# Kernel optimization log

Hardware: AMD Instinct MI355X
Metric: run time of the kernel (lower is better)

## Reference

```python
import jax, jax.numpy as jnp
import numpy as np

N = 20000   # atoms
E = 320000  # edges
G = 500     # molecules
D = 256     # node embedding depth
M = 128     # message depth
H = 4       # attention heads
DH = M // H
NR = 32     # radial basis functions
L = 4       # graph convolutions
T = 100     # atom types
EMB = 32    # atom type embedding dim
OUT = 512   # bottleneck dim
CUT = 6.0   # convolution cutoff (Angstrom)


def seg_softmax(logits, seg, num):
    m = jax.ops.segment_max(logits, seg, num_segments=num)
    e = jnp.exp(logits - m[seg])
    s = jax.ops.segment_sum(e, seg, num_segments=num)
    return e / (s[seg] + 1e-12)


def layernorm(x, eps=1e-5):
    mu = x.mean(-1, keepdims=True)
    var = ((x - mu) ** 2).mean(-1, keepdims=True)
    return (x - mu) * jax.lax.rsqrt(var + eps)


def setup_inputs() -> dict:
    key = jax.random.key(0)
    ks = jax.random.split(key, 20)
    s = 0.05
    pos = jax.random.normal(ks[0], (N, 3), dtype=jnp.float32) * 3.0
    z = jax.random.randint(ks[1], (N,), 0, T, dtype=jnp.int32)
    batch = jnp.sort(jax.random.randint(ks[2], (N,), 0, G, dtype=jnp.int32))
    edge_index = jax.random.randint(ks[3], (2, E), 0, N, dtype=jnp.int32)
    return {
        'pos': pos, 'z': z, 'batch': batch, 'edge_index': edge_index,
        'emb_table': jax.random.normal(ks[4], (T, EMB)) * s,
        'W_in': jax.random.normal(ks[5], (EMB + 3, D)) * s,
        'b_in': jnp.zeros((D,)),
        'Wq': jax.random.normal(ks[6], (L, D, M)) * s,
        'Wk': jax.random.normal(ks[7], (L, D, M)) * s,
        'Wv': jax.random.normal(ks[8], (L, D, M)) * s,
        'W_rbf': jax.random.normal(ks[9], (L, NR, M)) * s,
        'W_msg': jax.random.normal(ks[10], (L, M, D)) * s,
        'W_vgate': jax.random.normal(ks[11], (L, M, D)) * s,
        'W_vs': jax.random.normal(ks[12], (L, D, D)) * s,
        'W_node': jax.random.normal(ks[13], (L, D, D)) * s,
        'b_node': jnp.zeros((L, D)),
        'gamma': jnp.ones((L, D)),
        'w_att': jax.random.normal(ks[14], (D,)) * s,
        'W_out': jax.random.normal(ks[15], (D, OUT)) * s,
        'b_out': jnp.zeros((OUT,)),
    }


def reference(pos, z, batch, edge_index, emb_table, W_in, b_in, Wq, Wk, Wv,
              W_rbf, W_msg, W_vgate, W_vs, W_node, b_node, gamma, w_att,
              W_out, b_out):
    n = pos.shape[0]
    src, dst = edge_index[0], edge_index[1]
    # node init: atom-type embedding concat position -> linear
    h = jnp.concatenate([emb_table[z], pos], axis=-1) @ W_in + b_in  # [N,D]
    vfeat = jnp.zeros((n, 3, D), dtype=h.dtype)  # equivariant vector track
    # edge geometry + Bessel radial basis with cosine cutoff envelope
    rvec = pos[src] - pos[dst]                      # [E,3]
    dist = jnp.sqrt((rvec ** 2).sum(-1) + 1e-12)    # [E]
    unit = rvec / dist[:, None]
    freqs = jnp.arange(1, NR + 1, dtype=h.dtype) * (jnp.pi / CUT)
    env = jnp.where(dist < CUT, 0.5 * (jnp.cos(jnp.pi * dist / CUT) + 1.0), 0.0)
    rbf = jnp.sin(dist[:, None] * freqs) / dist[:, None] * env[:, None]  # [E,NR]
    inv_sqrt_dh = 1.0 / jnp.sqrt(jnp.asarray(DH, h.dtype))
    for l in range(L):
        ew = rbf @ W_rbf[l]                                   # [E,M] radial filter
        q = (h @ Wq[l])[dst].reshape(-1, H, DH)               # [E,H,DH]
        k = (h @ Wk[l])[src].reshape(-1, H, DH)
        vv = ((h @ Wv[l])[src] * ew).reshape(-1, H, DH)       # rbf-gated values
        logit = (q * k).sum(-1) * inv_sqrt_dh                 # [E,H]
        att = seg_softmax(logit, dst, n)                      # neighbor softmax per dest node
        me = (att[..., None] * vv).reshape(-1, M)             # [E,M] edge messages
        msg = jax.ops.segment_sum(me, dst, num_segments=n)    # [N,M]
        gate = me @ W_vgate[l]                                # [E,D]
        vfeat = vfeat + jax.ops.segment_sum(unit[:, :, None] * gate[:, None, :], dst, num_segments=n)
        upd = jax.nn.gelu(msg @ W_msg[l])                     # message -> node width
        upd = jax.nn.gelu(upd @ W_node[l] + b_node[l])        # nodewise FC layer
        vnorm = jnp.sqrt((vfeat ** 2).sum(1) + 1e-8)          # invariant vector norms [N,D]
        h = layernorm(h + upd + vnorm @ W_vs[l]) * gamma[l]
    # softmax graph aggregator -> bottleneck
    a = seg_softmax(h @ w_att, batch, G)                      # [N]
    pooled = jax.ops.segment_sum(a[:, None] * h, batch, num_segments=G)  # [G,D]
    return pooled @ W_out + b_out                             # [G,OUT]
```

## Files before the change

### kernel.cpp

```cpp
#include <hip/hip_runtime.h>
#include <math.h>

typedef unsigned char  u8;
typedef unsigned short u16;
typedef unsigned int   u32;
typedef __attribute__((ext_vector_type(8))) unsigned short ushort8;
typedef __attribute__((ext_vector_type(4))) unsigned short ushort4v;
typedef __attribute__((ext_vector_type(8))) short short8v;
typedef __attribute__((ext_vector_type(4))) float f32x4;
typedef __attribute__((ext_vector_type(2))) float f32x2;

__device__ __forceinline__ float gelu_f(float x) {
    const float c = 0.7978845608028654f;
    float x3 = x * x * x;
    float t = tanhf(c * (x + 0.044715f * x3));
    return 0.5f * x * (1.0f + t);
}

__device__ __forceinline__ u16 f2b(float f) {
    u32 u = __float_as_uint(f);
    return (u16)((u + 0x7FFFu + ((u >> 16) & 1u)) >> 16);
}
__device__ __forceinline__ float b2f(u16 u) {
    return __uint_as_float(((u32)u) << 16);
}

__device__ __forceinline__ u32 f2fp8_sw(float f) {
    u32 u = __float_as_uint(f);
    u32 s = (u >> 31) << 7;
    float af = fabsf(f);
    if (af >= 448.0f) return s | 0x7E;
    if (af < 0.015625f) {
        int m = __float2int_rn(af * 512.0f);
        if (m >= 8) return s | 0x08;
        return s | (u32)m;
    }
    u32 a = __float_as_uint(af);
    u32 r = a + 0xFFFFFu + ((a >> 20) & 1u);
    int e8 = (int)(r >> 23) - 120;
    u32 m3 = (r >> 20) & 7u;
    if (e8 >= 16) return s | 0x7E;
    return s | ((u32)e8 << 3) | m3;
}
__device__ __forceinline__ float fp8d_sw(u32 b) {
    u32 lo = b & 0x7Fu;
    u32 nb = (lo << 20) + 0x3C000000u;
    float n = __uint_as_float(nb | ((b & 0x80u) << 24));
    float sub = (float)(b & 7u) * 0.001953125f;
    sub = (b & 0x80u) ? -sub : sub;
    return (lo & 0x78u) ? n : sub;
}
__device__ __forceinline__ u8 f2fp8(float v) {
#if __has_builtin(__builtin_amdgcn_cvt_pk_fp8_f32)
    return (u8)(__builtin_amdgcn_cvt_pk_fp8_f32(v, v, 0, false) & 0xFF);
#else
    return (u8)f2fp8_sw(v);
#endif
}
__device__ __forceinline__ f32x2 kvdec(u32 pair) {
#if __has_builtin(__builtin_amdgcn_cvt_pk_f32_fp8)
    return __builtin_amdgcn_cvt_pk_f32_fp8((int)pair, false);
#else
    f32x2 r;
    r[0] = fp8d_sw(pair & 0xFF);
    r[1] = fp8d_sw((pair >> 8) & 0xFF);
    return r;
#endif
}

__device__ __forceinline__ void split_bf16(float f, u16& h, u16& l) {
    u32 u = __float_as_uint(f);
    u32 r = (u + 0x7FFFu + ((u >> 16) & 1u)) >> 16;
    h = (u16)r;
    float hf = __uint_as_float(r << 16);
    float d = f - hf;
    u32 u2 = __float_as_uint(d);
    l = (u16)((u2 + 0x7FFFu + ((u2 >> 16) & 1u)) >> 16);
}

__device__ __forceinline__ int xcd_swz(int orig, int nwg) {
    int q8 = nwg >> 3, r8 = nwg & 7;
    int xcd = orig & 7, ii = orig >> 3;
    return (xcd < r8 ? xcd * (q8 + 1) : r8 * (q8 + 1) + (xcd - r8) * q8) + ii;
}

__global__ __launch_bounds__(256) void zero2_i32(int* __restrict__ a, int na,
                                                 int* __restrict__ b, int nb) {
    int i = blockIdx.x * 256 + threadIdx.x;
    if (i < na) a[i] = 0;
    else if (i - na < nb) b[i - na] = 0;
}

struct TEntry { const float* src; u16* dh; u16* dl; int K; int N; };
struct TDesc  { TEntry e[29]; };

__global__ __launch_bounds__(256) void transpose_split(TDesc desc) {
    __shared__ float tile[32][33];
    TEntry en = desc.e[blockIdx.y];
    int tk = en.K >> 5, tn = en.N >> 5;
    int bx = blockIdx.x;
    if (bx >= tk * tn) return;
    int k0 = (bx % tk) * 32, n0 = (bx / tk) * 32;
    int tx = threadIdx.x & 31, ty = threadIdx.x >> 5;
    #pragma unroll
    for (int yy = 0; yy < 32; yy += 8)
        tile[ty + yy][tx] = en.src[(size_t)(k0 + ty + yy) * en.N + (n0 + tx)];
    __syncthreads();
    #pragma unroll
    for (int yy = 0; yy < 32; yy += 8) {
        int n = n0 + ty + yy, k = k0 + tx;
        float f = tile[tx][ty + yy];
        u16 h, l;
        split_bf16(f, h, l);
        en.dh[(size_t)n * en.K + k] = h;
        en.dl[(size_t)n * en.K + k] = l;
    }
}

__global__ __launch_bounds__(128) void build_rbf_table(
    const float* __restrict__ W_rbf, float* __restrict__ table)
{
    int k = blockIdx.x, l = blockIdx.y, m = threadIdx.x;
    const float* Wrbf_l = W_rbf + (size_t)l * 32 * 128;
    float* tbl = table + (size_t)l * 4098 * 128;
    const float PI = 3.14159265358979323846f;
    float d = fmaxf((float)k * (6.0f / 4096.0f), 1e-9f);
    float th = d * (PI / 6.0f);
    float s1, c1;
    __sincosf(th, &s1, &c1);
    float env = (d < 6.0f) ? (0.5f * c1 + 0.5f) : 0.0f;
    float invd = 1.0f / d;
    float two_c = 2.0f * c1;
    float sp = 0.f, sc = s1, dot = 0.f;
    #pragma unroll
    for (int r = 0; r < 32; ++r) {
        dot = fmaf(sc, Wrbf_l[r * 128 + m], dot);
        float sn = fmaf(two_c, sc, -sp);
        sp = sc; sc = sn;
    }
    tbl[(size_t)k * 128 + m] = dot * invd * env;
}

template<int OMODE, bool ACCUM, bool BIAS, bool DOGELU, bool SPLITB>
__global__ __launch_bounds__(256) void mfma_gemm(
    const u16* __restrict__ A, const u16* __restrict__ BH,
    const u16* __restrict__ BL, const float* __restrict__ bias,
    void* __restrict__ Cv, void* __restrict__ Cv2,
    int Mrows, int K, int Nc, int gx)
{
    constexpr bool STAGE_OUT = (OMODE == 1 || OMODE == 2);
    constexpr int MAIN_B = 128 * 40 * 2 * (SPLITB ? 3 : 2);
    constexpr int OUT_B  = STAGE_OUT ? 128 * 136 * 2 : 0;
    constexpr int SMEM_B = (MAIN_B > OUT_B) ? MAIN_B : OUT_B;
    __shared__ __align__(16) char smem[SMEM_B];
    u16 (*sA)[40]  = (u16(*)[40])smem;
    u16 (*sBh)[40] = (u16(*)[40])(smem + 128 * 40 * 2);
    u16 (*sBl)[40] = (u16(*)[40])(smem + 2 * 128 * 40 * 2);
    u16 (*sOut)[136] = (u16(*)[136])smem;

    const int wg = xcd_swz(blockIdx.x, gridDim.x);
    const int r0 = (wg / gx) * 128, c0 = (wg % gx) * 128;

    const int t = threadIdx.x;
    const int lane = t & 63, wid = t >> 6;
    const int wr = (wid >> 1) * 64, wc = (wid & 1) * 64;

    f32x4 acc[4][4] = {};

    const int srow = t >> 1;
    const int skc  = (t & 1) * 16;

    for (int k0 = 0; k0 < K; k0 += 32) {
        {
            int gr = r0 + srow;
            ushort8 h0, h1;
            if (gr < Mrows) {
                const u16* p = A + (size_t)gr * K + (k0 + skc);
                h0 = *(const ushort8*)p;
                h1 = *(const ushort8*)(p + 8);
            } else {
                #pragma unroll
                for (int j = 0; j < 8; ++j) { h0[j] = 0; h1[j] = 0; }
            }
            *(ushort8*)&sA[srow][skc]     = h0;
            *(ushort8*)&sA[srow][skc + 8] = h1;
        }
        {
            int cg = c0 + srow;
            const u16* ph = BH + (size_t)cg * K + (k0 + skc);
            *(ushort8*)&sBh[srow][skc]     = *(const ushort8*)(ph);
            *(ushort8*)&sBh[srow][skc + 8] = *(const ushort8*)(ph + 8);
            if constexpr (SPLITB) {
                const u16* pl = BL + (size_t)cg * K + (k0 + skc);
                *(ushort8*)&sBl[srow][skc]     = *(const ushort8*)(pl);
                *(ushort8*)&sBl[srow][skc + 8] = *(const ushort8*)(pl + 8);
            }
        }
        __syncthreads();

        const int arow = wr + (lane & 15);
        const int koff = (lane >> 4) * 8;
        short8v ah[4];
        #pragma unroll
        for (int fr = 0; fr < 4; ++fr)
            ah[fr] = *(const short8v*)&sA[arow + fr * 16][koff];
        #pragma unroll
        for (int fc = 0; fc < 4; ++fc) {
            int bcol = wc + fc * 16 + (lane & 15);
            short8v bh = *(const short8v*)&sBh[bcol][koff];
            #pragma unroll
            for (int fr = 0; fr < 4; ++fr)
                acc[fr][fc] = __builtin_amdgcn_mfma_f32_16x16x32_bf16(ah[fr], bh, acc[fr][fc], 0, 0, 0);
            if constexpr (SPLITB) {
                short8v bl = *(const short8v*)&sBl[bcol][koff];
                #pragma unroll
                for (int fr = 0; fr < 4; ++fr)
                    acc[fr][fc] = __builtin_amdgcn_mfma_f32_16x16x32_bf16(ah[fr], bl, acc[fr][fc], 0, 0, 0);
            }
        }
        __syncthreads();
    }

    if constexpr (STAGE_OUT) {
        #pragma unroll
        for (int fr = 0; fr < 4; ++fr) {
            int rbase = wr + fr * 16 + (lane >> 4) * 4;
            #pragma unroll
            for (int fc = 0; fc < 4; ++fc) {
                int col = wc + fc * 16 + (lane & 15);
                #pragma unroll
                for (int reg = 0; reg < 4; ++reg) {
                    float v = acc[fr][fc][reg];
                    if (BIAS)   v += bias[c0 + col];
                    if (DOGELU) v = gelu_f(v);
                    sOut[rbase + reg][col] = f2b(v);
                }
            }
        }
        __syncthreads();
        #pragma unroll
        for (int p = 0; p < 4; ++p) {
            int row = p * 32 + (t >> 3);
            int cch = (t & 7) * 16;
            int gr = r0 + row;
            if (gr < Mrows) {
                u16* gp = (u16*)Cv + (size_t)gr * Nc + c0 + cch;
                ushort8 v0 = *(ushort8*)&sOut[row][cch];
                ushort8 v1 = *(ushort8*)&sOut[row][cch + 8];
                if (OMODE == 2) {
                    ushort8 o0 = *(const ushort8*)gp;
                    ushort8 o1 = *(const ushort8*)(gp + 8);
                    #pragma unroll
                    for (int j = 0; j < 8; ++j) {
                        v0[j] = f2b(b2f(v0[j]) + b2f(o0[j]));
                        v1[j] = f2b(b2f(v1[j]) + b2f(o1[j]));
                    }
                }
                *(ushort8*)gp       = v0;
                *(ushort8*)(gp + 8) = v1;
            }
        }
    } else {
        #pragma unroll
        for (int fr = 0; fr < 4; ++fr) {
            int rbase = r0 + wr + fr * 16 + (lane >> 4) * 4;
            #pragma unroll
            for (int fc = 0; fc < 4; ++fc) {
                int col = c0 + wc + fc * 16 + (lane & 15);
                #pragma unroll
                for (int reg = 0; reg < 4; ++reg) {
                    int gr = rbase + reg;
                    if (gr >= Mrows) continue;
                    float v = acc[fr][fc][reg];
                    if (BIAS)   v += bias[col];
                    if (DOGELU) v = gelu_f(v);
                    if (OMODE == 0) {
                        float* pc = (float*)Cv + (size_t)gr * Nc + col;
                        if (ACCUM) v += *pc;
                        *pc = v;
                    } else {
                        if (col < 128)
                            ((u16*)Cv)[(size_t)gr * 128 + col] = f2b(v);
                        else if (col < 256)
                            ((u8*)Cv2)[(size_t)gr * 256 + (col - 128) * 2] = f2fp8(v);
                        else
                            ((u8*)Cv2)[(size_t)gr * 256 + (col - 256) * 2 + 1] = f2fp8(v);
                    }
                }
            }
        }
    }
}

__global__ __launch_bounds__(512) void mlp_kernel(
    const u16* __restrict__ msg, const u16* __restrict__ Wmsg,
    const u16* __restrict__ WndH, const u16* __restrict__ WndL,
    const float* __restrict__ bnd, u16* __restrict__ b2out, int Mrows)
{
    __shared__ __align__(16) u16 b1[128][264];
    __shared__ __align__(16) char sbuf[256 * 40 * 2 * 2];
    u16 (*sA)[40]   = (u16(*)[40])sbuf;
    u16 (*sB)[40]   = (u16(*)[40])(sbuf + 128 * 40 * 2);
    u16 (*sBh)[40]  = (u16(*)[40])sbuf;
    u16 (*sBl)[40]  = (u16(*)[40])(sbuf + 256 * 40 * 2);
    u16 (*sOut)[136] = (u16(*)[136])sbuf;

    const int r0 = xcd_swz(blockIdx.x, gridDim.x) * 128;
    const int t = threadIdx.x;
    const int lane = t & 63, wid = t >> 6;
    const int wr = (wid >> 2) * 64, wc = (wid & 3) * 64;

    f32x4 acc[4][4] = {};
    const int srowA = t >> 2, skcA = (t & 3) * 8;
    const int srowB = t >> 1, skcB = (t & 1) * 16;

    for (int k0 = 0; k0 < 128; k0 += 32) {
        {
            int gr = r0 + srowA;
            ushort8 h0;
            #pragma unroll
            for (int j = 0; j < 8; ++j) h0[j] = 0;
            if (gr < Mrows) h0 = *(const ushort8*)(msg + (size_t)gr * 128 + k0 + skcA);
            *(ushort8*)&sA[srowA][skcA] = h0;
        }
        {
            const u16* p = Wmsg + (size_t)srowB * 128 + k0 + skcB;
            *(ushort8*)&sB[srowB][skcB]     = *(const ushort8*)p;
            *(ushort8*)&sB[srowB][skcB + 8] = *(const ushort8*)(p + 8);
        }
        __syncthreads();
        const int arow = wr + (lane & 15);
        const int koff = (lane >> 4) * 8;
        short8v ah[4];
        #pragma unroll
        for (int fr = 0; fr < 4; ++fr)
            ah[fr] = *(const short8v*)&sA[arow + fr * 16][koff];
        #pragma unroll
        for (int fc = 0; fc < 4; ++fc) {
            int bcol = wc + fc * 16 + (lane & 15);
            short8v bh = *(const short8v*)&sB[bcol][koff];
            #pragma unroll
            for (int fr = 0; fr < 4; ++fr)
                acc[fr][fc] = __builtin_amdgcn_mfma_f32_16x16x32_bf16(ah[fr], bh, acc[fr][fc], 0, 0, 0);
        }
        __syncthreads();
    }
    #pragma unroll
    for (int fr = 0; fr < 4; ++fr) {
        int rbase = wr + fr * 16 + (lane >> 4) * 4;
        #pragma unroll
        for (int fc = 0; fc < 4; ++fc) {
            int col = wc + fc * 16 + (lane & 15);
            #pragma unroll
            for (int reg = 0; reg < 4; ++reg) {
                b1[rbase + reg][col] = f2b(gelu_f(acc[fr][fc][reg]));
                acc[fr][fc][reg] = 0.0f;
            }
        }
    }
    __syncthreads();

    for (int k0 = 0; k0 < 256; k0 += 32) {
        {
            const u16* ph = WndH + (size_t)srowB * 256 + k0 + skcB;
            const u16* pl = WndL + (size_t)srowB * 256 + k0 + skcB;
            *(ushort8*)&sBh[srowB][skcB]     = *(const ushort8*)ph;
            *(ushort8*)&sBh[srowB][skcB + 8] = *(const ushort8*)(ph + 8);
            *(ushort8*)&sBl[srowB][skcB]     = *(const ushort8*)pl;
            *(ushort8*)&sBl[srowB][skcB + 8] = *(const ushort8*)(pl + 8);
        }
        __syncthreads();
        const int arow = wr + (lane & 15);
        const int koff = (lane >> 4) * 8;
        short8v ah[4];
        #pragma unroll
        for (int fr = 0; fr < 4; ++fr)
            ah[fr] = *(const short8v*)&b1[arow + fr * 16][k0 + koff];
        #pragma unroll
        for (int fc = 0; fc < 4; ++fc) {
            int bcol = wc + fc * 16 + (lane & 15);
            short8v bh = *(const short8v*)&sBh[bcol][koff];
            short8v bl = *(const short8v*)&sBl[bcol][koff];
            #pragma unroll
            for (int fr = 0; fr < 4; ++fr) {
                acc[fr][fc] = __builtin_amdgcn_mfma_f32_16x16x32_bf16(ah[fr], bh, acc[fr][fc], 0, 0, 0);
                acc[fr][fc] = __builtin_amdgcn_mfma_f32_16x16x32_bf16(ah[fr], bl, acc[fr][fc], 0, 0, 0);
            }
        }
        __syncthreads();
    }

    #pragma unroll
    for (int fr = 0; fr < 4; ++fr) {
        int rbase = wr + fr * 16 + (lane >> 4) * 4;
        #pragma unroll
        for (int fc = 0; fc < 4; ++fc) {
            int col = wc + fc * 16 + (lane & 15);
            #pragma unroll
            for (int reg = 0; reg < 4; ++reg)
                sOut[rbase + reg][col] = f2b(gelu_f(acc[fr][fc][reg] + bnd[col]));
        }
    }
    __syncthreads();
    #pragma unroll
    for (int p = 0; p < 2; ++p) {
        int row = p * 64 + (t >> 3);
        int cch = (t & 7) * 16;
        int gr = r0 + row;
        if (gr < Mrows) {
            u16* gp = b2out + (size_t)gr * 256 + cch;
            *(ushort8*)gp       = *(ushort8*)&sOut[row][cch];
            *(ushort8*)(gp + 8) = *(ushort8*)&sOut[row][cch + 8];
        }
    }
}

__global__ __launch_bounds__(512) void vs_ln_kernel(
    const u16* __restrict__ vf, const u16* __restrict__ BH,
    const u16* __restrict__ BL, const u16* __restrict__ b2,
    const float* __restrict__ gamma_l, u16* __restrict__ h16, int Mrows)
{
    __shared__ __align__(16) u16 sA [128][40];
    __shared__ __align__(16) u16 sBh[256][40];
    __shared__ __align__(16) u16 sBl[256][40];
    __shared__ float sSum[128][4];
    __shared__ float sSq [128][4];

    const int r0 = blockIdx.x * 128;
    const int t = threadIdx.x;
    const int lane = t & 63, wid = t >> 6;
    const int wr = (wid >> 2) * 64, wc = (wid & 3) * 64;

    f32x4 acc[4][4] = {};
    const int K = 256;
    const int srow = t >> 2;
    const int skc  = (t & 3) * 8;

    for (int k0 = 0; k0 < K; k0 += 32) {
        {
            int gr = r0 + srow;
            ushort8 h0;
            #pragma unroll
            for (int j = 0; j < 8; ++j) h0[j] = 0;
            if (gr < Mrows) {
                const u16* base = vf + ((size_t)gr * 3) * 256 + k0 + skc;
                ushort8 v0 = *(const ushort8*)(base);
                ushort8 v1 = *(const ushort8*)(base + 256);
                ushort8 v2 = *(const ushort8*)(base + 512);
                #pragma unroll
                for (int j = 0; j < 8; ++j) {
                    float a = b2f(v0[j]), b = b2f(v1[j]), c = b2f(v2[j]);
                    h0[j] = f2b(sqrtf(a * a + b * b + c * c + 1e-8f));
                }
            }
            *(ushort8*)&sA[srow][skc] = h0;
        }
        {
            *(ushort8*)&sBh[srow][skc]       = *(const ushort8*)(BH + (size_t)srow * K + k0 + skc);
            *(ushort8*)&sBh[srow + 128][skc] = *(const ushort8*)(BH + (size_t)(srow + 128) * K + k0 + skc);
            *(ushort8*)&sBl[srow][skc]       = *(const ushort8*)(BL + (size_t)srow * K + k0 + skc);
            *(ushort8*)&sBl[srow + 128][skc] = *(const ushort8*)(BL + (size_t)(srow + 128) * K + k0 + skc);
        }
        __syncthreads();

        const int arow = wr + (lane & 15);
        const int koff = (lane >> 4) * 8;
        short8v ah[4];
        #pragma unroll
        for (int fr = 0; fr < 4; ++fr)
            ah[fr] = *(const short8v*)&sA[arow + fr * 16][koff];
        #pragma unroll
        for (int fc = 0; fc < 4; ++fc) {
            int bcol = wc + fc * 16 + (lane & 15);
            short8v bh = *(const short8v*)&sBh[bcol][koff];
            short8v bl = *(const short8v*)&sBl[bcol][koff];
            #pragma unroll
            for (int fr = 0; fr < 4; ++fr) {
                acc[fr][fc] = __builtin_amdgcn_mfma_f32_16x16x32_bf16(ah[fr], bh, acc[fr][fc], 0, 0, 0);
                acc[fr][fc] = __builtin_amdgcn_mfma_f32_16x16x32_bf16(ah[fr], bl, acc[fr][fc], 0, 0, 0);
            }
        }
        __syncthreads();
    }

    float psum[4][4] = {}, psq[4][4] = {};
    #pragma unroll
    for (int fr = 0; fr < 4; ++fr) {
        #pragma unroll
        for (int fc = 0; fc < 4; ++fc) {
            int col = wc + fc * 16 + (lane & 15);
            #pragma unroll
            for (int reg = 0; reg < 4; ++reg) {
                int gr = r0 + wr + fr * 16 + (lane >> 4) * 4 + reg;
                float x = 0.f;
                if (gr < Mrows) {
                    size_t ix = (size_t)gr * 256 + col;
                    x = acc[fr][fc][reg] + b2f(b2[ix]) + b2f(h16[ix]);
                }
                acc[fr][fc][reg] = x;
                psum[fr][reg] += x;
                psq[fr][reg]  = fmaf(x, x, psq[fr][reg]);
            }
        }
    }
    #pragma unroll
    for (int fr = 0; fr < 4; ++fr) {
        #pragma unroll
        for (int reg = 0; reg < 4; ++reg) {
            float s = psum[fr][reg], sq = psq[fr][reg];
            #pragma unroll
            for (int off = 8; off; off >>= 1) {
                s  += __shfl_xor(s, off);
                sq += __shfl_xor(sq, off);
            }
            psum[fr][reg] = s; psq[fr][reg] = sq;
        }
    }
    if ((lane & 15) == 0) {
        int qg = lane >> 4;
        #pragma unroll
        for (int fr = 0; fr < 4; ++fr) {
            #pragma unroll
            for (int reg = 0; reg < 4; ++reg) {
                int row = wr + fr * 16 + qg * 4 + reg;
                sSum[row][wc >> 6] = psum[fr][reg];
                sSq [row][wc >> 6] = psq[fr][reg];
            }
        }
    }
    __syncthreads();
    #pragma unroll
    for (int fr = 0; fr < 4; ++fr) {
        #pragma unroll
        for (int reg = 0; reg < 4; ++reg) {
            int row = wr + fr * 16 + (lane >> 4) * 4 + reg;
            int gr = r0 + row;
            if (gr >= Mrows) continue;
            float S = sSum[row][0] + sSum[row][1] + sSum[row][2] + sSum[row][3];
            float Q = sSq[row][0] + sSq[row][1] + sSq[row][2] + sSq[row][3];
            float mu = S * (1.0f / 256.0f);
            float var = fmaxf(Q * (1.0f / 256.0f) - mu * mu, 0.0f);
            float rs = rsqrtf(var + 1e-5f);
            #pragma unroll
            for (int fc = 0; fc < 4; ++fc) {
                int col = wc + fc * 16 + (lane & 15);
                float y = (acc[fr][fc][reg] - mu) * rs * gamma_l[col];
                h16[(size_t)gr * 256 + col] = f2b(y);
            }
        }
    }
}

__global__ __launch_bounds__(256) void setup_edges(
    const int* __restrict__ ei, const int* __restrict__ batch,
    const float* __restrict__ pos, int E_, int Nn,
    int* __restrict__ deg, int* __restrict__ gcnt, float4* __restrict__ eg)
{
    int x = blockIdx.x * 256 + threadIdx.x;
    if (x < E_) {
        int s = ei[x], dn = ei[E_ + x];
        atomicAdd(&deg[dn], 1);
        float dx = pos[s * 3 + 0] - pos[dn * 3 + 0];
        float dy = pos[s * 3 + 1] - pos[dn * 3 + 1];
        float dz = pos[s * 3 + 2] - pos[dn * 3 + 2];
        float d = sqrtf(dx * dx + dy * dy + dz * dz + 1e-12f);
        float invd = 1.0f / d;
        eg[x] = make_float4(dx * invd, dy * invd, dz * invd, d);
    }
    if (x < Nn) atomicAdd(&gcnt[batch[x]], 1);
}

__global__ __launch_bounds__(1024) void scan2_kernel(
    const int* __restrict__ cntA, int nA, int* __restrict__ outA, int* __restrict__ curA,
    const int* __restrict__ cntB, int nB, int* __restrict__ outB)
{
    __shared__ int part[1024];
    const int* cnt = (blockIdx.x == 0) ? cntA : cntB;
    int n          = (blockIdx.x == 0) ? nA : nB;
    int* out       = (blockIdx.x == 0) ? outA : outB;
    int* cursor    = (blockIdx.x == 0) ? curA : (int*)nullptr;
    int t = threadIdx.x;
    int chunk = (n + 1023) / 1024;
    int base = t * chunk;
    int s = 0;
    for (int k = 0; k < chunk; ++k) { int i = base + k; if (i < n) s += cnt[i]; }
    part[t] = s;
    __syncthreads();
    for (int off = 1; off < 1024; off <<= 1) {
        int u = (t >= off) ? part[t - off] : 0;
        __syncthreads();
        part[t] += u;
        __syncthreads();
    }
    int run = part[t] - s;
    for (int k = 0; k < chunk; ++k) {
        int i = base + k;
        if (i < n) {
            out[i] = run;
            if (cursor) cursor[i] = run;
            run += cnt[i];
        }
    }
    if (t == 1023) out[n] = part[1023];
}

__global__ void scatter_kernel(const int* __restrict__ ei, int* __restrict__ cursor,
                               int2* __restrict__ perm2, int E_) {
    int e = blockIdx.x * 256 + threadIdx.x;
    if (e < E_) {
        int p = atomicAdd(&cursor[ei[E_ + e]], 1);
        perm2[p] = make_int2(e, ei[e]);
    }
}

__global__ __launch_bounds__(256) void init_h_kernel(
    const int* __restrict__ z, const float* __restrict__ pos,
    const float* __restrict__ emb, const float* __restrict__ W_in,
    const float* __restrict__ b_in, u16* __restrict__ h16)
{
    int i = blockIdx.x, d = threadIdx.x;
    float acc = b_in[d];
    int zi = z[i];
    #pragma unroll 8
    for (int k = 0; k < 32; ++k)
        acc += emb[zi * 32 + k] * W_in[k * 256 + d];
    #pragma unroll
    for (int x = 0; x < 3; ++x)
        acc += pos[i * 3 + x] * W_in[(32 + x) * 256 + d];
    h16[(size_t)i * 256 + d] = f2b(acc);
}

__global__ __launch_bounds__(128) void edge_attn_kernel(
    const int* __restrict__ rowptr, const int2* __restrict__ perm2,
    const u16* __restrict__ q16, const u16* __restrict__ kv8,
    const float4* __restrict__ eg, const float* __restrict__ table_l,
    u16* __restrict__ msg, u16* __restrict__ U)
{
    int m = threadIdx.x;
    int i = blockIdx.x;

    int p0 = rowptr[i], p1 = rowptr[i + 1];
    float q = b2f(q16[(size_t)i * 128 + m]);
    float Mx = -1e30f, S = 0.f, am = 0.f, a0 = 0.f, a1 = 0.f, a2 = 0.f;
    const float iscale = 0.1767766952966369f;

    for (int p = p0; p < p1; p += 8) {
        int rem = p1 - p;
        int ee[8], jj[8];
        #pragma unroll
        for (int u = 0; u < 8; ++u) {
            int pp = p + (u < rem ? u : 0);
            int2 pe = perm2[pp];
            ee[u] = __builtin_amdgcn_readfirstlane(pe.x);
            jj[u] = __builtin_amdgcn_readfirstlane(pe.y);
        }
        u32 kv[8];
        float4 g[8];
        #pragma unroll
        for (int u = 0; u < 8; ++u) {
            kv[u] = kv8[(size_t)jj[u] * 128 + m];
            g[u]  = eg[ee[u]];
        }
        float lg[8], vd[8];
        #pragma unroll
        for (int u = 0; u < 8; ++u) {
            f32x2 c = kvdec(kv[u]);
            vd[u] = c[1];
            float pr = q * c[0];
            #pragma unroll
            for (int off = 16; off; off >>= 1) pr += __shfl_xor(pr, off);
            lg[u] = pr * iscale;
        }
        float ew[8];
        #pragma unroll
        for (int u = 0; u < 8; ++u) {
            float x = fminf(g[u].w * (4096.0f / 6.0f), 4096.0f);
            int b = (int)x;
            float tf = x - (float)b;
            float f0 = table_l[(size_t)b * 128 + m];
            float f1 = table_l[(size_t)(b + 1) * 128 + m];
            ew[u] = fmaf(tf, f1 - f0, f0);
        }
        float Mb = Mx;
        #pragma unroll
        for (int u = 0; u < 8; ++u) Mb = fmaxf(Mb, lg[u]);
        float sc = __expf(Mx - Mb);
        float w[8];
        #pragma unroll
        for (int u = 0; u < 8; ++u)
            w[u] = (u < rem) ? __expf(lg[u] - Mb) : 0.f;
        float ws = 0.f, wvs = 0.f, wx = 0.f, wy = 0.f, wz = 0.f;
        #pragma unroll
        for (int u = 0; u < 8; ++u) {
            float wv = w[u] * vd[u] * ew[u];
            ws  += w[u];
            wvs += wv;
            wx = fmaf(wv, g[u].x, wx);
            wy = fmaf(wv, g[u].y, wy);
            wz = fmaf(wv, g[u].z, wz);
        }
        S  = S  * sc + ws;
        am = am * sc + wvs;
        a0 = a0 * sc + wx;
        a1 = a1 * sc + wy;
        a2 = a2 * sc + wz;
        Mx = Mb;
    }
    float inv = 1.0f / (S + 1e-12f);
    msg[(size_t)i * 128 + m] = f2b(am * inv);
    U[((size_t)i * 3 + 0) * 128 + m] = f2b(a0 * inv);
    U[((size_t)i * 3 + 1) * 128 + m] = f2b(a1 * inv);
    U[((size_t)i * 3 + 2) * 128 + m] = f2b(a2 * inv);
}

__global__ __launch_bounds__(256) void pool_kernel(
    const u16* __restrict__ h16, const float* __restrict__ w_att,
    const int* __restrict__ gptr, u16* __restrict__ pooled)
{
    __shared__ float sM[4], sS[4];
    __shared__ float sAcc[4][256];
    int g = blockIdx.x;
    int t = threadIdx.x, w = t >> 6, lane = t & 63;
    int c0 = lane * 4;
    int n0 = gptr[g], n1 = gptr[g + 1];
    float4 wa = *(const float4*)(w_att + c0);
    float M = -1e30f, S = 0.f, a0 = 0.f, a1 = 0.f, a2 = 0.f, a3 = 0.f;
    for (int i = n0 + w; i < n1; i += 4) {
        ushort4v hv = *(const ushort4v*)(h16 + (size_t)i * 256 + c0);
        float h0 = b2f(hv[0]), h1 = b2f(hv[1]), h2 = b2f(hv[2]), h3 = b2f(hv[3]);
        float p = h0 * wa.x + h1 * wa.y + h2 * wa.z + h3 * wa.w;
        #pragma unroll
        for (int off = 32; off; off >>= 1) p += __shfl_xor(p, off);
        float nM = fmaxf(M, p);
        float sc = __expf(M - nM), wg = __expf(p - nM);
        S = S * sc + wg;
        a0 = a0 * sc + wg * h0;
        a1 = a1 * sc + wg * h1;
        a2 = a2 * sc + wg * h2;
        a3 = a3 * sc + wg * h3;
        M = nM;
    }
    sAcc[w][c0 + 0] = a0; sAcc[w][c0 + 1] = a1;
    sAcc[w][c0 + 2] = a2; sAcc[w][c0 + 3] = a3;
    if (lane == 0) { sM[w] = M; sS[w] = S; }
    __syncthreads();
    if (w == 0) {
        float Mg = fmaxf(fmaxf(sM[0], sM[1]), fmaxf(sM[2], sM[3]));
        float e0 = __expf(sM[0] - Mg), e1 = __expf(sM[1] - Mg);
        float e2 = __expf(sM[2] - Mg), e3 = __expf(sM[3] - Mg);
        float St = sS[0] * e0 + sS[1] * e1 + sS[2] * e2 + sS[3] * e3;
        float inv = 1.0f / (St + 1e-12f);
        #pragma unroll
        for (int c = 0; c < 4; ++c) {
            float v = sAcc[0][c0 + c] * e0 + sAcc[1][c0 + c] * e1
                    + sAcc[2][c0 + c] * e2 + sAcc[3][c0 + c] * e3;
            pooled[(size_t)g * 256 + c0 + c] = f2b(v * inv);
        }
    }
}

extern "C" void kernel_launch(void* const* d_in, const int* in_sizes, int n_in,
                              void* d_out, int out_size, void* d_ws, size_t ws_size,
                              hipStream_t stream)
{
    const float* pos   = (const float*)d_in[0];
    const int*   z     = (const int*)d_in[1];
    const int*   batch = (const int*)d_in[2];
    const int*   ei    = (const int*)d_in[3];
    const float* emb   = (const float*)d_in[4];
    const float* W_in  = (const float*)d_in[5];
    const float* b_in  = (const float*)d_in[6];
    const float* Wq    = (const float*)d_in[7];
    const float* Wk    = (const float*)d_in[8];
    const float* Wv    = (const float*)d_in[9];
    const float* W_rbf = (const float*)d_in[10];
    const float* W_msg = (const float*)d_in[11];
    const float* W_vg  = (const float*)d_in[12];
    const float* W_vs  = (const float*)d_in[13];
    const float* W_nd  = (const float*)d_in[14];
    const float* b_nd  = (const float*)d_in[15];
    const float* gam   = (const float*)d_in[16];
    const float* watt  = (const float*)d_in[17];
    const float* W_out = (const float*)d_in[18];
    const float* b_out = (const float*)d_in[19];

    const int N = in_sizes[0] / 3;
    const int E = in_sizes[3] / 2;
    const int G = out_size / 512;

    char* ws = (char*)d_ws;
    size_t o = 0;
    auto alloc = [&](size_t bytes) -> char* {
        o = (o + 255) & ~(size_t)255;
        char* r = ws + o;
        o += bytes;
        return r;
    };
    float4* f_eg   = (float4*)alloc((size_t)E * 16);
    u16*   h16     = (u16*)  alloc((size_t)N * 256 * 2);
    u16*   vf16    = (u16*)  alloc((size_t)N * 3 * 256 * 2);
    u16*   q16     = (u16*)  alloc((size_t)N * 128 * 2);
    u16*   kv8     = (u16*)  alloc((size_t)N * 128 * 2);
    u16*   umb     = (u16*)  alloc((size_t)N * 4 * 128 * 2);
    u16*   b2_16   = (u16*)  alloc((size_t)N * 256 * 2);
    u16*   pool16  = (u16*)  alloc((size_t)G * 256 * 2);
    float* f_table = (float*)alloc((size_t)4 * 4098 * 128 * 4);
    const size_t LS = 384 * 256 + 2 * (256 * 128) + 2 * (256 * 256);
    const size_t OFF_QKV = 0, OFF_VG = 384 * 256, OFF_MSG = OFF_VG + 256 * 128,
                 OFF_ND = OFF_MSG + 256 * 128, OFF_VS = OFF_ND + 256 * 256;
    const size_t OFF_OUT = LS * 4;
    u16* whi = (u16*)alloc((LS * 4 + 512 * 256) * sizeof(u16));
    u16* wlo = (u16*)alloc((LS * 4 + 512 * 256) * sizeof(u16));
    int*  i_deg   = (int*)alloc((size_t)N * 4);
    int*  i_rowp  = (int*)alloc((size_t)(N + 1) * 4);
    int*  i_cur   = (int*)alloc((size_t)(N + 1) * 4);
    int2* i_perm2 = (int2*)alloc((size_t)E * 8);
    int*  i_gcnt  = (int*)alloc((size_t)G * 4);
    int*  i_gptr  = (int*)alloc((size_t)(G + 1) * 4);

    u16* U16   = umb;
    u16* msg16 = umb + (size_t)3 * N * 128;

    TDesc td;
    int idx = 0;
    for (int l = 0; l < 4; ++l) {
        u16* bh = whi + (size_t)l * LS;
        u16* bl = wlo + (size_t)l * LS;
        td.e[idx++] = { Wq   + (size_t)l * 256 * 128, bh + OFF_QKV,             bl + OFF_QKV,             256, 128 };
        td.e[idx++] = { Wk   + (size_t)l * 256 * 128, bh + OFF_QKV + 128 * 256, bl + OFF_QKV + 128 * 256, 256, 128 };
        td.e[idx++] = { Wv   + (size_t)l * 256 * 128, bh + OFF_QKV + 256 * 256, bl + OFF_QKV + 256 * 256, 256, 128 };
        td.e[idx++] = { W_vg + (size_t)l * 128 * 256, bh + OFF_VG,  bl + OFF_VG,  128, 256 };
        td.e[idx++] = { W_msg+ (size_t)l * 128 * 256, bh + OFF_MSG, bl + OFF_MSG, 128, 256 };
        td.e[idx++] = { W_nd + (size_t)l * 256 * 256, bh + OFF_ND,  bl + OFF_ND,  256, 256 };
        td.e[idx++] = { W_vs + (size_t)l * 256 * 256, bh + OFF_VS,  bl + OFF_VS,  256, 256 };
    }
    td.e[idx++] = { W_out, whi + OFF_OUT, wlo + OFF_OUT, 256, 512 };

    zero2_i32<<<(N + G + 255) / 256, 256, 0, stream>>>(i_deg, N, i_gcnt, G);
    transpose_split<<<dim3(128, 29), 256, 0, stream>>>(td);
    build_rbf_table<<<dim3(4098, 4), 128, 0, stream>>>(W_rbf, f_table);

    setup_edges<<<(E + 255) / 256, 256, 0, stream>>>(ei, batch, pos, E, N,
                                                     i_deg, i_gcnt, f_eg);
    scan2_kernel<<<2, 1024, 0, stream>>>(i_deg, N, i_rowp, i_cur, i_gcnt, G, i_gptr);
    scatter_kernel<<<(E + 255) / 256, 256, 0, stream>>>(ei, i_cur, i_perm2, E);
    init_h_kernel<<<N, 256, 0, stream>>>(z, pos, emb, W_in, b_in, h16);

    const int MB  = (N + 127) / 128;
    const int MB3 = (3 * N + 127) / 128;
    const int MBG = (G + 127) / 128;

    for (int l = 0; l < 4; ++l) {
        u16* bh = whi + (size_t)l * LS;
        u16* bl = wlo + (size_t)l * LS;
        const float* bnd_l = b_nd + (size_t)l * 256;
        const float* gam_l = gam  + (size_t)l * 256;
        const float* tbl_l = f_table + (size_t)l * 4098 * 128;

        mfma_gemm<3,false,false,false,false><<<3 * MB, 256, 0, stream>>>(
            h16, bh + OFF_QKV, nullptr, nullptr, q16, kv8, N, 256, 384, 3);

        edge_attn_kernel<<<N, 128, 0, stream>>>(i_rowp, i_perm2, q16, kv8,
                                                f_eg, tbl_l, msg16, U16);

        if (l == 0)
            mfma_gemm<1,false,false,false,false><<<2 * MB3, 256, 0, stream>>>(
                U16, bh + OFF_VG, nullptr, nullptr, vf16, nullptr, 3 * N, 128, 256, 2);
        else
            mfma_gemm<2,false,false,false,false><<<2 * MB3, 256, 0, stream>>>(
                U16, bh + OFF_VG, nullptr, nullptr, vf16, nullptr, 3 * N, 128, 256, 2);

        mlp_kernel<<<MB, 512, 0, stream>>>(
            msg16, bh + OFF_MSG, bh + OFF_ND, bl + OFF_ND, bnd_l, b2_16, N);

        vs_ln_kernel<<<MB, 512, 0, stream>>>(
            vf16, bh + OFF_VS, bl + OFF_VS, b2_16, gam_l, h16, N);
    }

    pool_kernel<<<G, 256, 0, stream>>>(h16, watt, i_gptr, pool16);
    mfma_gemm<0,false,true,false,true><<<4 * MBG, 256, 0, stream>>>(
        pool16, whi + OFF_OUT, wlo + OFF_OUT, b_out, (float*)d_out, nullptr, G, 256, 512, 4);
}
```

Measured before the change: 785.6 us.

## Pack edge geometry into CSR records and bf16 paired RBF table, unroll 16

Edge geometry (distance and unit vector) is now computed during the CSR scatter and stored in a 16-byte record alongside the source index, so the attention kernel no longer does an indirect gather into a per-edge geometry array. The RBF lookup table is rebuilt as bf16 pairs (value at k and k+1 packed in one u32), halving table reads for interpolation. The edge loop is unrolled to 16 to raise memory-level parallelism. The trade-off is reduced precision for unit vectors and RBF weights, plus higher register pressure from the wider unroll.

```diff
diff --git a/kernel.cpp b/kernel.cpp
--- a/kernel.cpp
+++ b/kernel.cpp
@@ -117,12 +117,7 @@
     }
 }
 
-__global__ __launch_bounds__(128) void build_rbf_table(
-    const float* __restrict__ W_rbf, float* __restrict__ table)
-{
-    int k = blockIdx.x, l = blockIdx.y, m = threadIdx.x;
-    const float* Wrbf_l = W_rbf + (size_t)l * 32 * 128;
-    float* tbl = table + (size_t)l * 4098 * 128;
+__device__ __forceinline__ float rbf_val(int k, const float* __restrict__ Wrbf_l, int m) {
     const float PI = 3.14159265358979323846f;
     float d = fmaxf((float)k * (6.0f / 4096.0f), 1e-9f);
     float th = d * (PI / 6.0f);
@@ -138,7 +133,17 @@
         float sn = fmaf(two_c, sc, -sp);
         sp = sc; sc = sn;
     }
-    tbl[(size_t)k * 128 + m] = dot * invd * env;
+    return dot * invd * env;
+}
+
+__global__ __launch_bounds__(128) void build_rbf_table(
+    const float* __restrict__ W_rbf, u32* __restrict__ table)
+{
+    int k = blockIdx.x, l = blockIdx.y, m = threadIdx.x;
+    const float* Wrbf_l = W_rbf + (size_t)l * 32 * 128;
+    float v0 = rbf_val(k, Wrbf_l, m);
+    float v1 = rbf_val(k + 1, Wrbf_l, m);
+    table[((size_t)l * 4097 + k) * 128 + m] = (u32)f2b(v0) | ((u32)f2b(v1) << 16);
 }
 
 template<int OMODE, bool ACCUM, bool BIAS, bool DOGELU, bool SPLITB>
@@ -551,22 +556,12 @@
     }
 }
 
-__global__ __launch_bounds__(256) void setup_edges(
-    const int* __restrict__ ei, const int* __restrict__ batch,
-    const float* __restrict__ pos, int E_, int Nn,
-    int* __restrict__ deg, int* __restrict__ gcnt, float4* __restrict__ eg)
+__global__ __launch_bounds__(256) void setup_hist(
+    const int* __restrict__ ei, const int* __restrict__ batch, int E_, int Nn,
+    int* __restrict__ deg, int* __restrict__ gcnt)
 {
     int x = blockIdx.x * 256 + threadIdx.x;
-    if (x < E_) {
-        int s = ei[x], dn = ei[E_ + x];
-        atomicAdd(&deg[dn], 1);
-        float dx = pos[s * 3 + 0] - pos[dn * 3 + 0];
-        float dy = pos[s * 3 + 1] - pos[dn * 3 + 1];
-        float dz = pos[s * 3 + 2] - pos[dn * 3 + 2];
-        float d = sqrtf(dx * dx + dy * dy + dz * dz + 1e-12f);
-        float invd = 1.0f / d;
-        eg[x] = make_float4(dx * invd, dy * invd, dz * invd, d);
-    }
+    if (x < E_) atomicAdd(&deg[ei[E_ + x]], 1);
     if (x < Nn) atomicAdd(&gcnt[batch[x]], 1);
 }
 
@@ -604,12 +599,20 @@
     if (t == 1023) out[n] = part[1023];
 }
 
-__global__ void scatter_kernel(const int* __restrict__ ei, int* __restrict__ cursor,
-                               int2* __restrict__ perm2, int E_) {
+__global__ void scatter_kernel(const int* __restrict__ ei, const float* __restrict__ pos,
+                               int* __restrict__ cursor, int4* __restrict__ recs, int E_) {
     int e = blockIdx.x * 256 + threadIdx.x;
     if (e < E_) {
-        int p = atomicAdd(&cursor[ei[E_ + e]], 1);
-        perm2[p] = make_int2(e, ei[e]);
+        int s = ei[e], dn = ei[E_ + e];
+        int p = atomicAdd(&cursor[dn], 1);
+        float dx = pos[s * 3 + 0] - pos[dn * 3 + 0];
+        float dy = pos[s * 3 + 1] - pos[dn * 3 + 1];
+        float dz = pos[s * 3 + 2] - pos[dn * 3 + 2];
+        float d = sqrtf(dx * dx + dy * dy + dz * dz + 1e-12f);
+        float invd = 1.0f / d;
+        u32 uxy = (u32)f2b(dx * invd) | ((u32)f2b(dy * invd) << 16);
+        u32 uz  = (u32)f2b(dz * invd);
+        recs[p] = make_int4(s, __float_as_int(d), (int)uxy, (int)uz);
     }
 }
 
@@ -631,9 +634,9 @@
 }
 
 __global__ __launch_bounds__(128) void edge_attn_kernel(
-    const int* __restrict__ rowptr, const int2* __restrict__ perm2,
+    const int* __restrict__ rowptr, const int4* __restrict__ recs,
     const u16* __restrict__ q16, const u16* __restrict__ kv8,
-    const float4* __restrict__ eg, const float* __restrict__ table_l,
+    const u32* __restrict__ table_l,
     u16* __restrict__ msg, u16* __restrict__ U)
 {
     int m = threadIdx.x;
@@ -644,60 +647,61 @@
     float Mx = -1e30f, S = 0.f, am = 0.f, a0 = 0.f, a1 = 0.f, a2 = 0.f;
     const float iscale = 0.1767766952966369f;
 
-    for (int p = p0; p < p1; p += 8) {
+    for (int p = p0; p < p1; p += 16) {
         int rem = p1 - p;
-        int ee[8], jj[8];
-        #pragma unroll
-        for (int u = 0; u < 8; ++u) {
+        int jj[16];
+        float dd[16], ux[16], uy[16], uz[16];
+        #pragma unroll
+        for (int u = 0; u < 16; ++u) {
             int pp = p + (u < rem ? u : 0);
-            int2 pe = perm2[pp];
-            ee[u] = __builtin_amdgcn_readfirstlane(pe.x);
-            jj[u] = __builtin_amdgcn_readfirstlane(pe.y);
-        }
-        u32 kv[8];
-        float4 g[8];
-        #pragma unroll
-        for (int u = 0; u < 8; ++u) {
+            int4 r = recs[pp];
+            jj[u] = __builtin_amdgcn_readfirstlane(r.x);
+            dd[u] = __int_as_float(__builtin_amdgcn_readfirstlane(r.y));
+            u32 xy = (u32)__builtin_amdgcn_readfirstlane(r.z);
+            u32 zz = (u32)__builtin_amdgcn_readfirstlane(r.w);
+            ux[u] = b2f((u16)(xy & 0xFFFF));
+            uy[u] = b2f((u16)(xy >> 16));
+            uz[u] = b2f((u16)(zz & 0xFFFF));
+        }
+        u32 kv[16];
+        #pragma unroll
+        for (int u = 0; u < 16; ++u)
             kv[u] = kv8[(size_t)jj[u] * 128 + m];
-            g[u]  = eg[ee[u]];
-        }
-        float lg[8], vd[8];
-        #pragma unroll
-        for (int u = 0; u < 8; ++u) {
+        float ew[16];
+        #pragma unroll
+        for (int u = 0; u < 16; ++u) {
+            float x = fminf(dd[u] * (4096.0f / 6.0f), 4096.0f);
+            int b = (int)x;
+            float tf = x - (float)b;
+            u32 pr = table_l[(size_t)b * 128 + m];
+            float f0 = b2f((u16)(pr & 0xFFFF));
+            float f1 = b2f((u16)(pr >> 16));
+            ew[u] = fmaf(tf, f1 - f0, f0);
+        }
+        float lg[16], vd[16];
+        #pragma unroll
+        for (int u = 0; u < 16; ++u) {
             f32x2 c = kvdec(kv[u]);
             vd[u] = c[1];
-            float pr = q * c[0];
-            #pragma unroll
-            for (int off = 16; off; off >>= 1) pr += __shfl_xor(pr, off);
-            lg[u] = pr * iscale;
-        }
-        float ew[8];
-        #pragma unroll
-        for (int u = 0; u < 8; ++u) {
-            float x = fminf(g[u].w * (4096.0f / 6.0f), 4096.0f);
-            int b = (int)x;
-            float tf = x - (float)b;
-            float f0 = table_l[(size_t)b * 128 + m];
-            float f1 = table_l[(size_t)(b + 1) * 128 + m];
-            ew[u] = fmaf(tf, f1 - f0, f0);
+            float pr2 = q * c[0];
+            #pragma unroll
+            for (int off = 16; off; off >>= 1) pr2 += __shfl_xor(pr2, off);
+            lg[u] = pr2 * iscale;
         }
         float Mb = Mx;
         #pragma unroll
-        for (int u = 0; u < 8; ++u) Mb = fmaxf(Mb, lg[u]);
+        for (int u = 0; u < 16; ++u) Mb = fmaxf(Mb, lg[u]);
         float sc = __expf(Mx - Mb);
-        float w[8];
-        #pragma unroll
-        for (int u = 0; u < 8; ++u)
-            w[u] = (u < rem) ? __expf(lg[u] - Mb) : 0.f;
         float ws = 0.f, wvs = 0.f, wx = 0.f, wy = 0.f, wz = 0.f;
         #pragma unroll
-        for (int u = 0; u < 8; ++u) {
-            float wv = w[u] * vd[u] * ew[u];
-            ws  += w[u];
+        for (int u = 0; u < 16; ++u) {
+            float w = (u < rem) ? __expf(lg[u] - Mb) : 0.f;
+            float wv = w * vd[u] * ew[u];
+            ws  += w;
             wvs += wv;
-            wx = fmaf(wv, g[u].x, wx);
-            wy = fmaf(wv, g[u].y, wy);
-            wz = fmaf(wv, g[u].z, wz);
+            wx = fmaf(wv, ux[u], wx);
+            wy = fmaf(wv, uy[u], wy);
+            wz = fmaf(wv, uz[u], wz);
         }
         S  = S  * sc + ws;
         am = am * sc + wvs;
@@ -796,7 +800,6 @@
         o += bytes;
         return r;
     };
-    float4* f_eg   = (float4*)alloc((size_t)E * 16);
     u16*   h16     = (u16*)  alloc((size_t)N * 256 * 2);
     u16*   vf16    = (u16*)  alloc((size_t)N * 3 * 256 * 2);
     u16*   q16     = (u16*)  alloc((size_t)N * 128 * 2);
@@ -804,7 +807,7 @@
     u16*   umb     = (u16*)  alloc((size_t)N * 4 * 128 * 2);
     u16*   b2_16   = (u16*)  alloc((size_t)N * 256 * 2);
     u16*   pool16  = (u16*)  alloc((size_t)G * 256 * 2);
-    float* f_table = (float*)alloc((size_t)4 * 4098 * 128 * 4);
+    u32*   f_table = (u32*)  alloc((size_t)4 * 4097 * 128 * 4);
     const size_t LS = 384 * 256 + 2 * (256 * 128) + 2 * (256 * 256);
     const size_t OFF_QKV = 0, OFF_VG = 384 * 256, OFF_MSG = OFF_VG + 256 * 128,
                  OFF_ND = OFF_MSG + 256 * 128, OFF_VS = OFF_ND + 256 * 256;
@@ -814,7 +817,7 @@
     int*  i_deg   = (int*)alloc((size_t)N * 4);
     int*  i_rowp  = (int*)alloc((size_t)(N + 1) * 4);
     int*  i_cur   = (int*)alloc((size_t)(N + 1) * 4);
-    int2* i_perm2 = (int2*)alloc((size_t)E * 8);
+    int4* i_recs  = (int4*)alloc((size_t)E * 16);
     int*  i_gcnt  = (int*)alloc((size_t)G * 4);
     int*  i_gptr  = (int*)alloc((size_t)(G + 1) * 4);
 
@@ -838,12 +841,11 @@
 
     zero2_i32<<<(N + G + 255) / 256, 256, 0, stream>>>(i_deg, N, i_gcnt, G);
     transpose_split<<<dim3(128, 29), 256, 0, stream>>>(td);
-    build_rbf_table<<<dim3(4098, 4), 128, 0, stream>>>(W_rbf, f_table);
-
-    setup_edges<<<(E + 255) / 256, 256, 0, stream>>>(ei, batch, pos, E, N,
-                                                     i_deg, i_gcnt, f_eg);
+    build_rbf_table<<<dim3(4097, 4), 128, 0, stream>>>(W_rbf, f_table);
+
+    setup_hist<<<(E + 255) / 256, 256, 0, stream>>>(ei, batch, E, N, i_deg, i_gcnt);
     scan2_kernel<<<2, 1024, 0, stream>>>(i_deg, N, i_rowp, i_cur, i_gcnt, G, i_gptr);
-    scatter_kernel<<<(E + 255) / 256, 256, 0, stream>>>(ei, i_cur, i_perm2, E);
+    scatter_kernel<<<(E + 255) / 256, 256, 0, stream>>>(ei, pos, i_cur, i_recs, E);
     init_h_kernel<<<N, 256, 0, stream>>>(z, pos, emb, W_in, b_in, h16);
 
     const int MB  = (N + 127) / 128;
@@ -855,13 +857,13 @@
         u16* bl = wlo + (size_t)l * LS;
         const float* bnd_l = b_nd + (size_t)l * 256;
         const float* gam_l = gam  + (size_t)l * 256;
-        const float* tbl_l = f_table + (size_t)l * 4098 * 128;
+        const u32*   tbl_l = f_table + (size_t)l * 4097 * 128;
 
         mfma_gemm<3,false,false,false,false><<<3 * MB, 256, 0, stream>>>(
             h16, bh + OFF_QKV, nullptr, nullptr, q16, kv8, N, 256, 384, 3);
 
-        edge_attn_kernel<<<N, 128, 0, stream>>>(i_rowp, i_perm2, q16, kv8,
-                                                f_eg, tbl_l, msg16, U16);
+        edge_attn_kernel<<<N, 128, 0, stream>>>(i_rowp, i_recs, q16, kv8,
+                                                tbl_l, msg16, U16);
 
         if (l == 0)
             mfma_gemm<1,false,false,false,false><<<2 * MB3, 256, 0, stream>>>(
```

Measured after the change: 843.6 us. 7.4% more time.
